# Performance work log

Measured on AMD Instinct MI355X. Metric: run time of the kernel, lower is better.

The kernel has to match this reference:

```python
import jax, jax.numpy as jnp
import numpy as np

D_MODEL = 1024
D_FF = 4096
NUM_HEADS = 16
HEAD_DIM = D_MODEL // NUM_HEADS
THETA = 10000.0
EPS = 1e-5


def _trunc_init(key, shape):
    fan_in, fan_out = shape
    sigma = (2.0 / (fan_in + fan_out)) ** 0.5
    return sigma * jax.random.truncated_normal(key, -3.0, 3.0, shape, dtype=jnp.float32)


def setup_inputs() -> dict:
    key = jax.random.key(0)
    ks = jax.random.split(key, 8)
    x = jax.random.normal(ks[0], (2, 2048, D_MODEL), dtype=jnp.float32)
    return {
        "x": x,
        "Wq": _trunc_init(ks[1], (D_MODEL, D_MODEL)),
        "Wk": _trunc_init(ks[2], (D_MODEL, D_MODEL)),
        "Wv": _trunc_init(ks[3], (D_MODEL, D_MODEL)),
        "Wo": _trunc_init(ks[4], (D_MODEL, D_MODEL)),
        "g1": jnp.ones((D_MODEL,), dtype=jnp.float32),
        "g2": jnp.ones((D_MODEL,), dtype=jnp.float32),
        "W1": _trunc_init(ks[5], (D_MODEL, D_FF)),
        "W2": _trunc_init(ks[6], (D_FF, D_MODEL)),
        "W3": _trunc_init(ks[7], (D_MODEL, D_FF)),
    }


def _rmsnorm(x, g):
    xf = x.astype(jnp.float32)
    rms = jnp.sqrt(jnp.mean(xf * xf, axis=-1, keepdims=True) + EPS)
    return (xf / rms * g).astype(x.dtype)


def _rope(x, cos, sin):
    # x: [B, H, S, Dh]; cos/sin: [S, Dh//2]
    x1 = x[..., 0::2]
    x2 = x[..., 1::2]
    o1 = x1 * cos - x2 * sin
    o2 = x2 * cos + x1 * sin
    return jnp.stack([o1, o2], axis=-1).reshape(x.shape)


def reference(x, Wq, Wk, Wv, Wo, g1, g2, W1, W2, W3):
    B, S, _ = x.shape
    # --- attention branch ---
    h = _rmsnorm(x, g1)
    def split_heads(t):
        return t.reshape(B, S, NUM_HEADS, HEAD_DIM).transpose(0, 2, 1, 3)
    Q = split_heads(h @ Wq)
    K = split_heads(h @ Wk)
    V = split_heads(h @ Wv)
    # RoPE
    powers = jnp.arange(0, HEAD_DIM, 2, dtype=jnp.float32) / HEAD_DIM
    inv_freq = 1.0 / (THETA ** powers)
    t = jnp.arange(S, dtype=jnp.float32)
    freqs = jnp.outer(t, inv_freq)  # [S, Dh//2]
    cos, sin = jnp.cos(freqs), jnp.sin(freqs)
    Q = _rope(Q, cos, sin)
    K = _rope(K, cos, sin)
    # scaled dot-product attention with causal mask
    scale = 1.0 / jnp.sqrt(jnp.float32(HEAD_DIM))
    scores = jnp.einsum('bhqd,bhkd->bhqk', Q, K) * scale
    causal = jnp.tril(jnp.ones((S, S), dtype=bool))
    scores = jnp.where(causal, scores, -jnp.inf)
    attn = jax.nn.softmax(scores, axis=-1)
    ctx = jnp.einsum('bhqk,bhkd->bhqd', attn, V)
    ctx = ctx.transpose(0, 2, 1, 3).reshape(B, S, D_MODEL)
    out1 = x + ctx @ Wo
    # --- FFN branch (SwiGLU) ---
    h2 = _rmsnorm(out1, g2)
    x1 = h2 @ W1
    x3 = h2 @ W3
    ffn = (x1 * jax.nn.sigmoid(x1) * x3) @ W2
    return out1 + ffn
```

## Files before the change

kernel.cpp:

```cpp
#include <hip/hip_runtime.h>
#include <math.h>

typedef unsigned short ushort_t;
typedef __attribute__((ext_vector_type(8))) short short8;
typedef __attribute__((ext_vector_type(4))) float f32x4;

#define MFMA16(a, b, c) __builtin_amdgcn_mfma_f32_16x16x32_bf16((a), (b), (c), 0, 0, 0)

static __device__ __forceinline__ float fast_exp2(float x) {
#if __has_builtin(__builtin_amdgcn_exp2f)
  return __builtin_amdgcn_exp2f(x);
#else
  return exp2f(x);
#endif
}

static __device__ __forceinline__ ushort_t f2bf(float f) {
  unsigned int u = __float_as_uint(f);
  u = u + 0x7FFFu + ((u >> 16) & 1u);
  return (ushort_t)(u >> 16);
}
static __device__ __forceinline__ float bf2f(ushort_t s) {
  return __uint_as_float(((unsigned int)s) << 16);
}

static __device__ __forceinline__ void stage16(const ushort_t* g_perlane, char* l_uniform, int lane) {
#if __has_builtin(__builtin_amdgcn_global_load_lds)
  __builtin_amdgcn_global_load_lds((const __attribute__((address_space(1))) void*)g_perlane,
                                   (__attribute__((address_space(3))) void*)l_uniform, 16, 0, 0);
#else
  *(uint4*)(l_uniform + lane * 16) = *(const uint4*)g_perlane;
#endif
}

__global__ __launch_bounds__(256) void rmsnorm_k(const float* __restrict__ x,
                                                 const float* __restrict__ g,
                                                 ushort_t* __restrict__ o) {
  const int r = blockIdx.x, t = threadIdx.x;
  const float4 xv = ((const float4*)(x + (size_t)r * 1024))[t];
  float ss = xv.x * xv.x + xv.y * xv.y + xv.z * xv.z + xv.w * xv.w;
#pragma unroll
  for (int m = 32; m >= 1; m >>= 1) ss += __shfl_xor(ss, m);
  __shared__ float wp[4];
  if ((t & 63) == 0) wp[t >> 6] = ss;
  __syncthreads();
  const float inv = rsqrtf((wp[0] + wp[1] + wp[2] + wp[3]) * (1.f / 1024.f) + 1e-5f);
  const float4 gv = ((const float4*)g)[t];
  ushort4 ov = {f2bf(xv.x * inv * gv.x), f2bf(xv.y * inv * gv.y),
                f2bf(xv.z * inv * gv.z), f2bf(xv.w * inv * gv.w)};
  *(ushort4*)(o + (size_t)r * 1024 + t * 4) = ov;
}

__global__ __launch_bounds__(256) void transpose_cast_k(const float* __restrict__ in,
                                                        ushort_t* __restrict__ out,
                                                        int R, int C, int mode) {
  __shared__ ushort_t Ts[64][72];
  const int t = threadIdx.x;
  const int c0 = blockIdx.x * 64, r0 = blockIdx.y * 64;
  const int lr = t >> 4, lc = (t & 15) * 4;
#pragma unroll
  for (int i = 0; i < 4; ++i) {
    const float4 v = *(const float4*)&in[(size_t)(r0 + lr + i * 16) * C + c0 + lc];
    Ts[lr + i * 16][lc + 0] = f2bf(v.x);
    Ts[lr + i * 16][lc + 1] = f2bf(v.y);
    Ts[lr + i * 16][lc + 2] = f2bf(v.z);
    Ts[lr + i * 16][lc + 3] = f2bf(v.w);
  }
  __syncthreads();
  const int rr = (t & 15) * 4;
#pragma unroll
  for (int i = 0; i < 4; ++i) {
    const int cc = (t >> 4) + i * 16;
    const int cg = c0 + cc;
    int orow;
    if (mode == 0)
      orow = cg;
    else
      orow = ((cg >> 7) << 8) + (((cg >> 4) & 7) << 5) + (cg & 15) + (mode == 2 ? 16 : 0);
    ushort4 o = {Ts[rr + 0][cc], Ts[rr + 1][cc], Ts[rr + 2][cc], Ts[rr + 3][cc]};
    *(ushort4*)&out[(size_t)orow * R + r0 + rr] = o;
  }
}

__global__ __launch_bounds__(256) void rope_k(ushort_t* __restrict__ buf, float scale) {
  const int idx = blockIdx.x * 256 + threadIdx.x;
  const int row = idx >> 7, rem = idx & 127;
  const int head = rem >> 3, gq = rem & 7;
  const int i0 = gq * 4;
  const int s = row & 2047;
  ushort_t* p = buf + (size_t)row * 3072 + head * 64 + i0 * 2;
  uint4 v = *(uint4*)p;
  ushort_t* e = (ushort_t*)&v;
#pragma unroll
  for (int k = 0; k < 4; ++k) {
    const float ang = (float)s * expf(-(float)(i0 + k) * 0.28782313662425572f);
    float sn, cs;
    sincosf(ang, &sn, &cs);
    const float x1 = bf2f(e[2 * k]), x2 = bf2f(e[2 * k + 1]);
    e[2 * k] = f2bf((x1 * cs - x2 * sn) * scale);
    e[2 * k + 1] = f2bf((x2 * cs + x1 * sn) * scale);
  }
  *(uint4*)p = v;
}

template <int FUSED>
__global__ __launch_bounds__(512, 2) void gemm256_k(const ushort_t* __restrict__ A,
                                                    const ushort_t* __restrict__ Bt,
                                                    ushort_t* __restrict__ C,
                                                    int N, int K) {
  __shared__ uint4 smem[131072 / 16];
  char* sm = (char*)smem;
  const int flat = blockIdx.y * gridDim.x + blockIdx.x;
  const int total = gridDim.x * gridDim.y;
  const int swz = (flat & 7) * (total >> 3) + (flat >> 3);
  const int bx = swz % gridDim.x, by = swz / gridDim.x;
  const int t = threadIdx.x, lane = t & 63, w = t >> 6;
  const int g = lane >> 4, li = lane & 15;
  const int wr = w >> 2, wc = w & 3;
  const int nr0 = bx * 256, m0 = by * 256;
  const int wb4 = (t & 448) << 4;
  const int srow = t & 255;
  const int sg0 = t >> 8;
  const size_t rowA = (size_t)(m0 + srow) * K;
  const size_t rowB = (size_t)(nr0 + srow) * K;
  f32x4 acc[8][4] = {};
  const int nkt = K >> 5;

  auto stageA = [&](int kt) {
    char* dA = sm + (kt & 3) * 16384;
    const int k0 = kt << 5;
#pragma unroll
    for (int c = 0; c < 2; ++c)
      stage16(A + rowA + k0 + (c * 2 + sg0) * 8, dA + ((c * 512) << 4) + wb4, lane);
  };
  auto stageB = [&](int kt) {
    char* dB = sm + 65536 + (kt & 3) * 16384;
    const int k0 = kt << 5;
#pragma unroll
    for (int c = 0; c < 2; ++c)
      stage16(Bt + rowB + k0 + (c * 2 + sg0) * 8, dB + ((c * 512) << 4) + wb4, lane);
  };

  stageA(0); stageB(0); stageA(1); stageB(1);
  asm volatile("s_waitcnt vmcnt(4)" ::: "memory");
  __builtin_amdgcn_s_barrier();
  for (int kt = 0; kt < nkt; ++kt) {
    const char* sA = sm + (kt & 3) * 16384;
    const char* sB = sm + 65536 + (kt & 3) * 16384;
    const bool pf = (kt + 2 < nkt);
    short8 af0[4], bfr[4];
#pragma unroll
    for (int mi = 0; mi < 4; ++mi)
      af0[mi] = *(const short8*)(sA + ((g * 256 + wr * 128 + mi * 16 + li) << 4));
#pragma unroll
    for (int ni = 0; ni < 4; ++ni)
      bfr[ni] = *(const short8*)(sB + ((g * 256 + wc * 64 + ni * 16 + li) << 4));
    if (pf) stageA(kt + 2);
    __builtin_amdgcn_s_barrier();
    __builtin_amdgcn_s_setprio(1);
#pragma unroll
    for (int mi = 0; mi < 4; ++mi)
#pragma unroll
      for (int ni = 0; ni < 4; ++ni) acc[mi][ni] = MFMA16(af0[mi], bfr[ni], acc[mi][ni]);
    __builtin_amdgcn_s_setprio(0);
    __builtin_amdgcn_s_barrier();
    short8 af1[4];
#pragma unroll
    for (int mi = 0; mi < 4; ++mi)
      af1[mi] = *(const short8*)(sA + ((g * 256 + wr * 128 + (mi + 4) * 16 + li) << 4));
    if (pf) stageB(kt + 2);
    if (pf)
      asm volatile("s_waitcnt vmcnt(4)" ::: "memory");
    else if (kt + 1 < nkt)
      asm volatile("s_waitcnt vmcnt(0)" ::: "memory");
    __builtin_amdgcn_s_barrier();
    __builtin_amdgcn_s_setprio(1);
#pragma unroll
    for (int mi = 0; mi < 4; ++mi)
#pragma unroll
      for (int ni = 0; ni < 4; ++ni) acc[mi + 4][ni] = MFMA16(af1[mi], bfr[ni], acc[mi + 4][ni]);
    __builtin_amdgcn_s_setprio(0);
    __builtin_amdgcn_s_barrier();
  }
  if (FUSED == 0) {
#pragma unroll
    for (int mi = 0; mi < 8; ++mi)
#pragma unroll
      for (int ni = 0; ni < 4; ++ni)
#pragma unroll
        for (int r = 0; r < 4; ++r) {
          const int row = m0 + wr * 128 + mi * 16 + g * 4 + r;
          const int col = nr0 + wc * 64 + ni * 16 + li;
          C[(size_t)row * N + col] = f2bf(acc[mi][ni][r]);
        }
  } else {
#pragma unroll
    for (int mi = 0; mi < 8; ++mi)
#pragma unroll
      for (int p = 0; p < 2; ++p)
#pragma unroll
        for (int r = 0; r < 4; ++r) {
          const float v1 = acc[mi][2 * p][r];
          const float v3 = acc[mi][2 * p + 1][r];
          const float o = v1 / (1.f + __expf(-v1)) * v3;
          const int row = m0 + wr * 128 + mi * 16 + g * 4 + r;
          const int col = bx * 128 + wc * 32 + p * 16 + li;
          C[(size_t)row * N + col] = f2bf(o);
        }
  }
}

template <int MODE, int SPLIT>
__global__ __launch_bounds__(256) void gemm_k(const ushort_t* __restrict__ A,
                                              const ushort_t* __restrict__ Bt,
                                              const float* __restrict__ R,
                                              void* __restrict__ C,
                                              int N, int K) {
  __shared__ uint4 smem[49152 / 16];
  char* sm = (char*)smem;
  const int flat = blockIdx.y * gridDim.x + blockIdx.x;
  const int total = gridDim.x * gridDim.y;
  const int swz = (flat & 7) * (total >> 3) + (flat >> 3);
  const int bx = swz % gridDim.x, by = swz / gridDim.x;
  const int t = threadIdx.x, lane = t & 63, w = t >> 6;
  const int g = lane >> 4, li = lane & 15;
  const int wr = w >> 1, wc = w & 1;
  const int n0 = bx * 128, m0 = by * 128;
  const int wb = t & 192;
  const int r0s = t & 127, g0s = (t >> 7) << 3;
  const int Ksl = K / SPLIT;
  const int kbase = blockIdx.z * Ksl;
  const size_t rowA = (size_t)(m0 + r0s) * K;
  const size_t rowB = (size_t)(n0 + r0s) * K;
  f32x4 acc[4][4] = {};
  const int nkt = Ksl >> 5;

  auto stage_all = [&](int buf, int kt) {
    const int k0 = kbase + (kt << 5) + g0s;
    char* dA = sm + buf * 8192;
    char* dB = sm + 24576 + buf * 8192;
    stage16(A + rowA + k0, dA + (wb << 4), lane);
    stage16(A + rowA + k0 + 16, dA + ((256 + wb) << 4), lane);
    stage16(Bt + rowB + k0, dB + (wb << 4), lane);
    stage16(Bt + rowB + k0 + 16, dB + ((256 + wb) << 4), lane);
  };

  stage_all(0, 0);
  stage_all(1, 1);
  asm volatile("s_waitcnt vmcnt(4)" ::: "memory");
  __builtin_amdgcn_s_barrier();
  int b0 = 0;
  for (int kt = 0; kt < nkt; ++kt) {
    int bn = b0 + 2;
    if (bn >= 3) bn -= 3;
    if (kt + 2 < nkt) stage_all(bn, kt + 2);
    const char* smA = sm + b0 * 8192;
    const char* smB = sm + 24576 + b0 * 8192;
    short8 af[4], bfr[4];
#pragma unroll
    for (int mi = 0; mi < 4; ++mi)
      af[mi] = *(const short8*)(smA + ((g * 128 + wr * 64 + mi * 16 + li) << 4));
#pragma unroll
    for (int ni = 0; ni < 4; ++ni)
      bfr[ni] = *(const short8*)(smB + ((g * 128 + wc * 64 + ni * 16 + li) << 4));
    __builtin_amdgcn_s_setprio(1);
#pragma unroll
    for (int mi = 0; mi < 4; ++mi)
#pragma unroll
      for (int ni = 0; ni < 4; ++ni) acc[mi][ni] = MFMA16(af[mi], bfr[ni], acc[mi][ni]);
    __builtin_amdgcn_s_setprio(0);
    if (kt + 2 < nkt) {
      asm volatile("s_waitcnt vmcnt(4) lgkmcnt(0)" ::: "memory");
      __builtin_amdgcn_s_barrier();
    } else if (kt + 1 < nkt) {
      asm volatile("s_waitcnt vmcnt(0) lgkmcnt(0)" ::: "memory");
      __builtin_amdgcn_s_barrier();
    }
    ++b0;
    if (b0 == 3) b0 = 0;
  }
#pragma unroll
  for (int mi = 0; mi < 4; ++mi)
#pragma unroll
    for (int ni = 0; ni < 4; ++ni)
#pragma unroll
      for (int r = 0; r < 4; ++r) {
        const int row = m0 + wr * 64 + mi * 16 + g * 4 + r;
        const int col = n0 + wc * 64 + ni * 16 + li;
        const float v = acc[mi][ni][r];
        if (MODE == 1)
          ((float*)C)[(size_t)row * N + col] = v + R[(size_t)row * N + col];
        else if (MODE == 2)
          atomicAdd(&((float*)C)[(size_t)row * N + col], v);
        else
          ((ushort_t*)C)[(size_t)row * N + col] = f2bf(v);
      }
}

__global__ __launch_bounds__(256) void attn_k(const ushort_t* __restrict__ qkv,
                                              ushort_t* __restrict__ ctx) {
  __shared__ uint4 smemv[32768 / 16];
  char* sm = (char*)smemv;
  const int qt = 31 - blockIdx.x;
  const int bh = blockIdx.y;
  const int b = bh >> 4, h = bh & 15;
  const int t = threadIdx.x, lane = t & 63, w = t >> 6;
  const int g = lane >> 4, li = lane & 15;
  const int rowb = b * 2048;
  const size_t qbase = (size_t)rowb * 3072 + h * 64;
  const int q0 = qt * 64;
  const ushort_t* kptr = qkv + qbase + 1024;
  const ushort_t* vptr = qkv + qbase + 2048;

  short8 qa[2];
  {
    const int qrow = q0 + w * 16 + li;
    qa[0] = *(const short8*)(qkv + qbase + (size_t)qrow * 3072 + 8 * g);
    qa[1] = *(const short8*)(qkv + qbase + (size_t)qrow * 3072 + 32 + 8 * g);
  }
  f32x4 acc[4] = {};
  float mr = -INFINITY, lr = 0.f;
  const int sb = g * 20;

  const int vj = t & 63;
  const int vcol2 = 2 * (((vj >> 5) << 5) + (((vj >> 2) & 3) << 3) + (((vj >> 4) & 1) << 2) + (vj & 3));

  uint4 vr0, vr1;
  auto stageK = [&](int buf, int kt) {
    char* dst = sm + buf * 8192;
    const ushort_t* src = kptr + (size_t)kt * 64 * 3072 + (size_t)(t & 63) * 3072;
    stage16(src + (t >> 6) * 8, dst + ((t & 192) << 4), lane);
    stage16(src + ((t >> 6) + 4) * 8, dst + 4096 + ((t & 192) << 4), lane);
  };
  auto loadV = [&](int kt) {
    const ushort_t* src = vptr + (size_t)(kt * 64 + vj) * 3072 + w * 16;
    vr0 = *(const uint4*)src;
    vr1 = *(const uint4*)(src + 8);
  };
  auto writeV = [&](int buf) {
    char* dst = sm + 16384 + buf * 8192;
    ushort_t tmp[16];
    *(uint4*)tmp = vr0;
    *(uint4*)(tmp + 8) = vr1;
#pragma unroll
    for (int e = 0; e < 16; ++e) {
      const int dh = w * 16 + e;
      *(ushort_t*)(dst + dh * 128 + (vcol2 ^ ((dh & 7) << 4))) = tmp[e];
    }
  };

  stageK(0, 0);
  loadV(0);
  writeV(0);
  __syncthreads();
  int cur = 0;
  for (int kt = 0; kt <= qt; ++kt) {
    if (kt < qt) {
      stageK(cur ^ 1, kt + 1);
      loadV(kt + 1);
    }
    const char* Kf = sm + cur * 8192;
    const char* Vt = sm + 16384 + cur * 8192;
    f32x4 s[4];
    __builtin_amdgcn_s_setprio(1);
#pragma unroll
    for (int nt = 0; nt < 4; ++nt) {
      f32x4 z = {0.f, 0.f, 0.f, 0.f};
#pragma unroll
      for (int hh = 0; hh < 2; ++hh) {
        const short8 kf = *(const short8*)(Kf + (((hh * 4 + g) * 64 + nt * 16 + li) << 4));
        z = MFMA16(kf, qa[hh], z);
      }
      s[nt] = z;
    }
    __builtin_amdgcn_s_setprio(0);
    if (kt == qt) {
      const int qq = q0 + w * 16 + li;
#pragma unroll
      for (int nt = 0; nt < 4; ++nt)
#pragma unroll
        for (int r = 0; r < 4; ++r)
          if (kt * 64 + nt * 16 + g * 4 + r > qq) s[nt][r] = -INFINITY;
    }
    float pm = -INFINITY;
#pragma unroll
    for (int nt = 0; nt < 4; ++nt)
#pragma unroll
      for (int r = 0; r < 4; ++r) pm = fmaxf(pm, s[nt][r]);
    pm = fmaxf(pm, __shfl_xor(pm, 16));
    pm = fmaxf(pm, __shfl_xor(pm, 32));
    if (__any(pm > mr + 11.5f)) {
      const float nm = fmaxf(mr, pm);
      const float rs = fast_exp2(mr - nm);
      mr = nm;
      lr *= rs;
#pragma unroll
      for (int r = 0; r < 4; ++r) {
        const float rsb = __shfl(rs, sb + r);
#pragma unroll
        for (int dt = 0; dt < 4; ++dt) acc[dt][r] *= rsb;
      }
    }
    float ps = 0.f;
#pragma unroll
    for (int nt = 0; nt < 4; ++nt)
#pragma unroll
      for (int r = 0; r < 4; ++r) {
        s[nt][r] = fast_exp2(s[nt][r] - mr);
        ps += s[nt][r];
      }
    ps += __shfl_xor(ps, 16);
    ps += __shfl_xor(ps, 32);
    lr += ps;
    if (kt < qt) writeV(cur ^ 1);
    short8 pa[2];
#pragma unroll
    for (int m = 0; m < 2; ++m)
#pragma unroll
      for (int r = 0; r < 4; ++r) {
        pa[m][r] = (short)f2bf(s[2 * m][r]);
        pa[m][4 + r] = (short)f2bf(s[2 * m + 1][r]);
      }
    __builtin_amdgcn_s_setprio(1);
#pragma unroll
    for (int dt = 0; dt < 4; ++dt) {
      const int dh = dt * 16 + li;
#pragma unroll
      for (int m = 0; m < 2; ++m) {
        const short8 vb = *(const short8*)(Vt + dh * 128 + ((m * 64 + g * 16) ^ ((dh & 7) << 4)));
        acc[dt] = MFMA16(pa[m], vb, acc[dt]);
      }
    }
    __builtin_amdgcn_s_setprio(0);
    __syncthreads();
    cur ^= 1;
  }
#pragma unroll
  for (int r = 0; r < 4; ++r) {
    const float lrb = __shfl(lr, sb + r);
    const float inv = 1.f / lrb;
    const int row = rowb + q0 + w * 16 + g * 4 + r;
#pragma unroll
    for (int dt = 0; dt < 4; ++dt) {
      const int col = h * 64 + dt * 16 + li;
      ctx[(size_t)row * 1024 + col] = f2bf(acc[dt][r] * inv);
    }
  }
}

extern "C" void kernel_launch(void* const* d_in, const int* in_sizes, int n_in,
                              void* d_out, int out_size, void* d_ws, size_t ws_size,
                              hipStream_t stream) {
  const float* x = (const float*)d_in[0];
  const float* Wq = (const float*)d_in[1];
  const float* Wk = (const float*)d_in[2];
  const float* Wv = (const float*)d_in[3];
  const float* Wo = (const float*)d_in[4];
  const float* g1 = (const float*)d_in[5];
  const float* g2 = (const float*)d_in[6];
  const float* W1 = (const float*)d_in[7];
  const float* W2 = (const float*)d_in[8];
  const float* W3 = (const float*)d_in[9];
  float* out = (float*)d_out;

  char* wsb = (char*)d_ws;
  ushort_t* hb = (ushort_t*)(wsb);
  ushort_t* qkv = (ushort_t*)(wsb + (8u << 20));
  ushort_t* ctx = (ushort_t*)(wsb + (32u << 20));
  ushort_t* x1b = (ushort_t*)(wsb + (8u << 20));
  ushort_t* wqkvT = (ushort_t*)(wsb + (72u << 20));
  ushort_t* woT = (ushort_t*)(wsb + (78u << 20));
  ushort_t* w13iT = (ushort_t*)(wsb + (80u << 20));
  ushort_t* w2T = (ushort_t*)(wsb + (96u << 20));

  transpose_cast_k<<<dim3(16, 16), 256, 0, stream>>>(Wq, wqkvT, 1024, 1024, 0);
  transpose_cast_k<<<dim3(16, 16), 256, 0, stream>>>(Wk, wqkvT + 1024 * 1024, 1024, 1024, 0);
  transpose_cast_k<<<dim3(16, 16), 256, 0, stream>>>(Wv, wqkvT + 2 * 1024 * 1024, 1024, 1024, 0);
  transpose_cast_k<<<dim3(16, 16), 256, 0, stream>>>(Wo, woT, 1024, 1024, 0);
  transpose_cast_k<<<dim3(64, 16), 256, 0, stream>>>(W1, w13iT, 1024, 4096, 1);
  transpose_cast_k<<<dim3(64, 16), 256, 0, stream>>>(W3, w13iT, 1024, 4096, 2);
  transpose_cast_k<<<dim3(16, 64), 256, 0, stream>>>(W2, w2T, 4096, 1024, 0);

  rmsnorm_k<<<4096, 256, 0, stream>>>(x, g1, hb);
  gemm_k<0, 1><<<dim3(24, 32), 256, 0, stream>>>(hb, wqkvT, nullptr, qkv, 3072, 1024);
  rope_k<<<2048, 256, 0, stream>>>(qkv, 0.125f * 1.44269504088896f);
  rope_k<<<2048, 256, 0, stream>>>(qkv + 1024, 1.0f);
  attn_k<<<dim3(32, 32), 256, 0, stream>>>(qkv, ctx);
  gemm_k<1, 1><<<dim3(8, 32), 256, 0, stream>>>(ctx, woT, x, out, 1024, 1024);
  rmsnorm_k<<<4096, 256, 0, stream>>>(out, g2, hb);
  gemm256_k<1><<<dim3(32, 16), 512, 0, stream>>>(hb, w13iT, x1b, 4096, 1024);
  gemm_k<1, 1><<<dim3(8, 32), 256, 0, stream>>>(x1b, w2T, out, out, 1024, 4096);
}
```

Before: 388.0 us.

## Split attention into 32-row query tiles with 2-wave blocks and truncate P to bf16

The attention kernel now uses 128-thread blocks that each handle a 32-row query tile, down from 64 rows, and launches twice as many blocks. Each thread stages more of the K and V tiles to make up for having fewer threads. The aim is more blocks for scheduling and better balance across the causal triangle. The cost is that each K/V tile is loaded twice as often per query row. Softmax probabilities are also converted to bf16 by truncation rather than rounding, which saves ALU work at a small accuracy cost.

New measurement: 408.2 us. 1.05x slower.

```diff
diff --git a/kernel.cpp b/kernel.cpp
--- a/kernel.cpp
+++ b/kernel.cpp
@@ -19,6 +19,9 @@
   unsigned int u = __float_as_uint(f);
   u = u + 0x7FFFu + ((u >> 16) & 1u);
   return (ushort_t)(u >> 16);
+}
+static __device__ __forceinline__ ushort_t f2bf_trunc(float f) {
+  return (ushort_t)(__float_as_uint(f) >> 16);
 }
 static __device__ __forceinline__ float bf2f(ushort_t s) {
   return __uint_as_float(((unsigned int)s) << 16);
@@ -297,18 +300,19 @@
       }
 }
 
-__global__ __launch_bounds__(256) void attn_k(const ushort_t* __restrict__ qkv,
+__global__ __launch_bounds__(128) void attn_k(const ushort_t* __restrict__ qkv,
                                               ushort_t* __restrict__ ctx) {
   __shared__ uint4 smemv[32768 / 16];
   char* sm = (char*)smemv;
-  const int qt = 31 - blockIdx.x;
+  const int qq = 63 - blockIdx.x;
   const int bh = blockIdx.y;
   const int b = bh >> 4, h = bh & 15;
   const int t = threadIdx.x, lane = t & 63, w = t >> 6;
   const int g = lane >> 4, li = lane & 15;
   const int rowb = b * 2048;
   const size_t qbase = (size_t)rowb * 3072 + h * 64;
-  const int q0 = qt * 64;
+  const int q0 = qq * 32;
+  const int ktmax = qq >> 1;
   const ushort_t* kptr = qkv + qbase + 1024;
   const ushort_t* vptr = qkv + qbase + 2048;
 
@@ -323,28 +327,32 @@
   const int sb = g * 20;
 
   const int vj = t & 63;
+  const int vd0 = (t >> 6) * 32;
   const int vcol2 = 2 * (((vj >> 5) << 5) + (((vj >> 2) & 3) << 3) + (((vj >> 4) & 1) << 2) + (vj & 3));
 
-  uint4 vr0, vr1;
+  uint4 vr[4];
   auto stageK = [&](int buf, int kt) {
     char* dst = sm + buf * 8192;
     const ushort_t* src = kptr + (size_t)kt * 64 * 3072 + (size_t)(t & 63) * 3072;
-    stage16(src + (t >> 6) * 8, dst + ((t & 192) << 4), lane);
-    stage16(src + ((t >> 6) + 4) * 8, dst + 4096 + ((t & 192) << 4), lane);
+#pragma unroll
+    for (int c = 0; c < 4; ++c) {
+      const int g8 = c * 2 + w;
+      stage16(src + g8 * 8, dst + g8 * 1024, lane);
+    }
   };
   auto loadV = [&](int kt) {
-    const ushort_t* src = vptr + (size_t)(kt * 64 + vj) * 3072 + w * 16;
-    vr0 = *(const uint4*)src;
-    vr1 = *(const uint4*)(src + 8);
+    const ushort_t* src = vptr + (size_t)(kt * 64 + vj) * 3072 + vd0;
+#pragma unroll
+    for (int c = 0; c < 4; ++c) vr[c] = *(const uint4*)(src + c * 8);
   };
   auto writeV = [&](int buf) {
     char* dst = sm + 16384 + buf * 8192;
-    ushort_t tmp[16];
-    *(uint4*)tmp = vr0;
-    *(uint4*)(tmp + 8) = vr1;
-#pragma unroll
-    for (int e = 0; e < 16; ++e) {
-      const int dh = w * 16 + e;
+    ushort_t tmp[32];
+#pragma unroll
+    for (int c = 0; c < 4; ++c) *(uint4*)(tmp + c * 8) = vr[c];
+#pragma unroll
+    for (int e = 0; e < 32; ++e) {
+      const int dh = vd0 + e;
       *(ushort_t*)(dst + dh * 128 + (vcol2 ^ ((dh & 7) << 4))) = tmp[e];
     }
   };
@@ -354,8 +362,8 @@
   writeV(0);
   __syncthreads();
   int cur = 0;
-  for (int kt = 0; kt <= qt; ++kt) {
-    if (kt < qt) {
+  for (int kt = 0; kt <= ktmax; ++kt) {
+    if (kt < ktmax) {
       stageK(cur ^ 1, kt + 1);
       loadV(kt + 1);
     }
@@ -374,13 +382,13 @@
       s[nt] = z;
     }
     __builtin_amdgcn_s_setprio(0);
-    if (kt == qt) {
-      const int qq = q0 + w * 16 + li;
+    if (kt == ktmax) {
+      const int qrow = q0 + w * 16 + li;
 #pragma unroll
       for (int nt = 0; nt < 4; ++nt)
 #pragma unroll
         for (int r = 0; r < 4; ++r)
-          if (kt * 64 + nt * 16 + g * 4 + r > qq) s[nt][r] = -INFINITY;
+          if (kt * 64 + nt * 16 + g * 4 + r > qrow) s[nt][r] = -INFINITY;
     }
     float pm = -INFINITY;
 #pragma unroll
@@ -412,14 +420,14 @@
     ps += __shfl_xor(ps, 16);
     ps += __shfl_xor(ps, 32);
     lr += ps;
-    if (kt < qt) writeV(cur ^ 1);
+    if (kt < ktmax) writeV(cur ^ 1);
     short8 pa[2];
 #pragma unroll
     for (int m = 0; m < 2; ++m)
 #pragma unroll
       for (int r = 0; r < 4; ++r) {
-        pa[m][r] = (short)f2bf(s[2 * m][r]);
-        pa[m][4 + r] = (short)f2bf(s[2 * m + 1][r]);
+        pa[m][r] = (short)f2bf_trunc(s[2 * m][r]);
+        pa[m][4 + r] = (short)f2bf_trunc(s[2 * m + 1][r]);
       }
     __builtin_amdgcn_s_setprio(1);
 #pragma unroll
@@ -485,7 +493,7 @@
   gemm_k<0, 1><<<dim3(24, 32), 256, 0, stream>>>(hb, wqkvT, nullptr, qkv, 3072, 1024);
   rope_k<<<2048, 256, 0, stream>>>(qkv, 0.125f * 1.44269504088896f);
   rope_k<<<2048, 256, 0, stream>>>(qkv + 1024, 1.0f);
-  attn_k<<<dim3(32, 32), 256, 0, stream>>>(qkv, ctx);
+  attn_k<<<dim3(64, 32), 128, 0, stream>>>(qkv, ctx);
   gemm_k<1, 1><<<dim3(8, 32), 256, 0, stream>>>(ctx, woT, x, out, 1024, 1024);
   rmsnorm_k<<<4096, 256, 0, stream>>>(out, g2, hb);
   gemm256_k<1><<<dim3(32, 16), 512, 0, stream>>>(hb, w13iT, x1b, 4096, 1024);
```

## Load attention K tiles directly into registers and truncate P to bf16

Applied to the files above, without the earlier changes.

The attention kernel no longer stages K tiles through LDS. Each lane now loads its K fragments straight from global memory into registers and double-buffers them (kc/kn), which halves the shared-memory footprint and removes the LDS reads for K. Separately, the softmax probabilities are converted to bf16 by truncation instead of round-to-nearest, saving a few ALU ops per element at some cost in accuracy. The trade-off is higher register pressure and uncoalesced, strided global loads for K.

Result: slower. 439.2 us (+13.2%).

```diff
diff --git a/kernel.cpp b/kernel.cpp
--- a/kernel.cpp
+++ b/kernel.cpp
@@ -19,6 +19,9 @@
   unsigned int u = __float_as_uint(f);
   u = u + 0x7FFFu + ((u >> 16) & 1u);
   return (ushort_t)(u >> 16);
+}
+static __device__ __forceinline__ ushort_t f2bf_trunc(float f) {
+  return (ushort_t)(__float_as_uint(f) >> 16);
 }
 static __device__ __forceinline__ float bf2f(ushort_t s) {
   return __uint_as_float(((unsigned int)s) << 16);
@@ -299,7 +302,7 @@
 
 __global__ __launch_bounds__(256) void attn_k(const ushort_t* __restrict__ qkv,
                                               ushort_t* __restrict__ ctx) {
-  __shared__ uint4 smemv[32768 / 16];
+  __shared__ uint4 smemv[16384 / 16];
   char* sm = (char*)smemv;
   const int qt = 31 - blockIdx.x;
   const int bh = blockIdx.y;
@@ -325,20 +328,25 @@
   const int vj = t & 63;
   const int vcol2 = 2 * (((vj >> 5) << 5) + (((vj >> 2) & 3) << 3) + (((vj >> 4) & 1) << 2) + (vj & 3));
 
+  const ushort_t* kfb = kptr + (size_t)li * 3072 + g * 8;
+  short8 kc[8], kn[8];
+  auto loadK = [&](int kt, short8* kr) {
+    const ushort_t* src = kfb + (size_t)kt * 64 * 3072;
+#pragma unroll
+    for (int nt = 0; nt < 4; ++nt)
+#pragma unroll
+      for (int hh = 0; hh < 2; ++hh)
+        kr[nt * 2 + hh] = *(const short8*)(src + nt * 16 * 3072 + hh * 32);
+  };
+
   uint4 vr0, vr1;
-  auto stageK = [&](int buf, int kt) {
-    char* dst = sm + buf * 8192;
-    const ushort_t* src = kptr + (size_t)kt * 64 * 3072 + (size_t)(t & 63) * 3072;
-    stage16(src + (t >> 6) * 8, dst + ((t & 192) << 4), lane);
-    stage16(src + ((t >> 6) + 4) * 8, dst + 4096 + ((t & 192) << 4), lane);
-  };
   auto loadV = [&](int kt) {
     const ushort_t* src = vptr + (size_t)(kt * 64 + vj) * 3072 + w * 16;
     vr0 = *(const uint4*)src;
     vr1 = *(const uint4*)(src + 8);
   };
   auto writeV = [&](int buf) {
-    char* dst = sm + 16384 + buf * 8192;
+    char* dst = sm + buf * 8192;
     ushort_t tmp[16];
     *(uint4*)tmp = vr0;
     *(uint4*)(tmp + 8) = vr1;
@@ -349,28 +357,24 @@
     }
   };
 
-  stageK(0, 0);
+  loadK(0, kc);
   loadV(0);
   writeV(0);
   __syncthreads();
   int cur = 0;
   for (int kt = 0; kt <= qt; ++kt) {
     if (kt < qt) {
-      stageK(cur ^ 1, kt + 1);
+      loadK(kt + 1, kn);
       loadV(kt + 1);
     }
-    const char* Kf = sm + cur * 8192;
-    const char* Vt = sm + 16384 + cur * 8192;
+    const char* Vt = sm + cur * 8192;
     f32x4 s[4];
     __builtin_amdgcn_s_setprio(1);
 #pragma unroll
     for (int nt = 0; nt < 4; ++nt) {
       f32x4 z = {0.f, 0.f, 0.f, 0.f};
-#pragma unroll
-      for (int hh = 0; hh < 2; ++hh) {
-        const short8 kf = *(const short8*)(Kf + (((hh * 4 + g) * 64 + nt * 16 + li) << 4));
-        z = MFMA16(kf, qa[hh], z);
-      }
+      z = MFMA16(kc[nt * 2], qa[0], z);
+      z = MFMA16(kc[nt * 2 + 1], qa[1], z);
       s[nt] = z;
     }
     __builtin_amdgcn_s_setprio(0);
@@ -418,8 +422,8 @@
     for (int m = 0; m < 2; ++m)
 #pragma unroll
       for (int r = 0; r < 4; ++r) {
-        pa[m][r] = (short)f2bf(s[2 * m][r]);
-        pa[m][4 + r] = (short)f2bf(s[2 * m + 1][r]);
+        pa[m][r] = (short)f2bf_trunc(s[2 * m][r]);
+        pa[m][4 + r] = (short)f2bf_trunc(s[2 * m + 1][r]);
       }
     __builtin_amdgcn_s_setprio(1);
 #pragma unroll
@@ -433,6 +437,10 @@
     }
     __builtin_amdgcn_s_setprio(0);
     __syncthreads();
+    if (kt < qt) {
+#pragma unroll
+      for (int i = 0; i < 8; ++i) kc[i] = kn[i];
+    }
     cur ^= 1;
   }
 #pragma unroll
```
